# Kernel tuning notes

Measured on AMD Instinct MI355X. Metric: run time of the kernel, lower is better.

Reference implementation:

```python
import jax, jax.numpy as jnp
import numpy as np

IN_FEATURES = 4096
OUT_FEATURES = 4096
B, S = 4, 2048


def setup_inputs() -> dict:
    key = jax.random.key(0)
    k_x, k_w, k_ws, k_ss, k_b = jax.random.split(key, 5)
    x = jax.random.normal(k_x, (B, S, IN_FEATURES), dtype=jnp.float32)
    weight_quantized = jax.random.randint(k_w, (OUT_FEATURES, IN_FEATURES), -128, 128, dtype=jnp.int32).astype(jnp.int8)
    # realistic per-output-channel weight scales (small positive)
    weight_scale = jax.random.uniform(k_ws, (OUT_FEATURES,), dtype=jnp.float32, minval=1e-3, maxval=2e-2)
    # smoothing scales near 1 (clamped to [0.01, 100] in from_float)
    smooth_scale = jax.random.uniform(k_ss, (IN_FEATURES,), dtype=jnp.float32, minval=0.5, maxval=2.0)
    bias = 0.01 * jax.random.normal(k_b, (OUT_FEATURES,), dtype=jnp.float32)
    return {"x": x, "weight_quantized": weight_quantized, "weight_scale": weight_scale,
            "smooth_scale": smooth_scale, "bias": bias}


def reference(x, weight_quantized, weight_scale, smooth_scale, bias):
    # per-tensor dynamic activation quantization after smooth-scale divide
    x_smooth = x / smooth_scale                                   # [B,S,in]
    act_scale = jnp.max(jnp.abs(x_smooth)) / 127.0                # scalar
    x_quant = jnp.clip(jnp.round(x_smooth / (act_scale + 1e-5)), -128, 127).astype(jnp.int8)
    # int8 GEMM emulated in fp32 (matches torch reference: F.linear on float casts)
    out = jnp.einsum('bsi,oi->bso', x_quant.astype(jnp.float32),
                     weight_quantized.astype(jnp.float32))        # [B,S,out]
    out = out * act_scale * weight_scale                          # fused dequant
    return out + bias
```

## Files before the change

kernel.cpp:

```cpp
#include <hip/hip_runtime.h>
#include <stdint.h>

#define M_TOT 8192
#define N_TOT 4096
#define K_TOT 4096

typedef int v4i __attribute__((ext_vector_type(4)));
typedef int v16i __attribute__((ext_vector_type(16)));

#define BM 256
#define BN 256
#define SUB 64
#define NS (K_TOT / SUB)
#define A_SUB (BM * SUB)
#define B_SUB (BN * SUB)
#define BUF_BYTES (A_SUB + B_SUB)

__global__ void prep_reduce(const int4* __restrict__ w32, int* __restrict__ w8,
                            int nw4, const float4* __restrict__ smooth4,
                            const float4* __restrict__ x,
                            unsigned int* __restrict__ maxbits, int nx4) {
  const int stride = gridDim.x * blockDim.x;
  const int g0 = blockIdx.x * blockDim.x + threadIdx.x;
  for (int i = g0; i < nw4; i += stride) {
    int4 v = w32[i];
    w8[i] = (v.x & 0xff) | ((v.y & 0xff) << 8) | ((v.z & 0xff) << 16) | (v.w << 24);
  }
  float4 s = smooth4[g0 & (K_TOT / 4 - 1)];
  const float rx = 1.0f / s.x, ry = 1.0f / s.y, rz = 1.0f / s.z, rw = 1.0f / s.w;
  float m = 0.0f;
  for (int i = g0; i < nx4; i += stride) {
    float4 v = x[i];
    m = fmaxf(m, fabsf(v.x * rx));
    m = fmaxf(m, fabsf(v.y * ry));
    m = fmaxf(m, fabsf(v.z * rz));
    m = fmaxf(m, fabsf(v.w * rw));
  }
#pragma unroll
  for (int off = 32; off; off >>= 1) m = fmaxf(m, __shfl_xor(m, off));
  __shared__ float sm[4];
  if ((threadIdx.x & 63) == 0) sm[threadIdx.x >> 6] = m;
  __syncthreads();
  if (threadIdx.x == 0) {
    float mm = fmaxf(fmaxf(sm[0], sm[1]), fmaxf(sm[2], sm[3]));
    atomicMax(maxbits, __float_as_uint(mm));
  }
}

__global__ void quantize_x(const float4* __restrict__ x,
                           const float4* __restrict__ smooth4,
                           const unsigned int* __restrict__ maxbits,
                           int* __restrict__ xq, int n4) {
  const float d = __uint_as_float(*maxbits) / 127.0f + 1e-5f;
  const float inv = 1.0f / d;
  const int stride = gridDim.x * blockDim.x;
  const int g0 = blockIdx.x * blockDim.x + threadIdx.x;
  float4 s = smooth4[g0 & (K_TOT / 4 - 1)];
  const float rx = inv / s.x, ry = inv / s.y, rz = inv / s.z, rw = inv / s.w;
  for (int i = g0; i < n4; i += stride) {
    float4 v = x[i];
    int q0 = (int)fminf(fmaxf(rintf(v.x * rx), -128.0f), 127.0f);
    int q1 = (int)fminf(fmaxf(rintf(v.y * ry), -128.0f), 127.0f);
    int q2 = (int)fminf(fmaxf(rintf(v.z * rz), -128.0f), 127.0f);
    int q3 = (int)fminf(fmaxf(rintf(v.w * rw), -128.0f), 127.0f);
    xq[i] = (q0 & 0xff) | ((q1 & 0xff) << 8) | ((q2 & 0xff) << 16) | (q3 << 24);
  }
}

__global__ __launch_bounds__(512, 2) void gemm_i8(
    const int8_t* __restrict__ Aq,
    const int8_t* __restrict__ Wt,
    const unsigned int* __restrict__ maxbits,
    const float* __restrict__ wscale,
    const float* __restrict__ bias,
    float* __restrict__ out) {
  __shared__ int8_t lds[4 * BUF_BYTES];

  const int tid = threadIdx.x;
  const int lane = tid & 63;
  const int wid = tid >> 6;
  const int l31 = lane & 31;
  const int lhi5 = lane >> 5;

  const int flat = blockIdx.y * gridDim.x + blockIdx.x;
  const int swz = (flat & 7) * 64 + (flat >> 3);
  const int m0 = (swz / (N_TOT / BN)) * BM;
  const int n0 = (swz % (N_TOT / BN)) * BN;

  const int wave_m = wid >> 2;
  const int wave_n = wid & 3;

  const int row_l = lane >> 2;
  const int gcol = ((lane & 3) ^ ((lane >> 3) & 3)) << 4;
  const int8_t* Abase = Aq + (size_t)m0 * K_TOT;
  const int8_t* Bbase = Wt + (size_t)n0 * K_TOT;
  int goff[2];
#pragma unroll
  for (int c = 0; c < 2; ++c) {
    int grow = (wid * 2 + c) * 16 + row_l;
    goff[c] = grow * K_TOT + gcol;
  }

  auto stage = [&](int dstbuf, int koff) {
#pragma unroll
    for (int c = 0; c < 2; ++c) {
      __builtin_amdgcn_global_load_lds(
          (const __attribute__((address_space(1))) void*)(Abase + goff[c] + koff),
          (__attribute__((address_space(3))) void*)(lds + dstbuf * BUF_BYTES + (wid * 2 + c) * 1024),
          16, 0, 0);
      __builtin_amdgcn_global_load_lds(
          (const __attribute__((address_space(1))) void*)(Bbase + goff[c] + koff),
          (__attribute__((address_space(3))) void*)(lds + dstbuf * BUF_BYTES + A_SUB + (wid * 2 + c) * 1024),
          16, 0, 0);
    }
  };

  const int f = (l31 >> 1) & 3;
  const int slot0 = ((0 + lhi5) ^ f) << 4;
  const int slot1 = ((2 + lhi5) ^ f) << 4;
  const int aBase = (wave_m * 128 + l31) * SUB;
  const int bBase = (wave_n * 64 + l31) * SUB;

  stage(0, 0);
  stage(1, SUB);
  stage(2, 2 * SUB);
  asm volatile("s_waitcnt vmcnt(8)" ::: "memory");
  __builtin_amdgcn_s_barrier();
  __builtin_amdgcn_sched_barrier(0);

  v16i acc[4][2] = {};

#pragma unroll 4
  for (int s = 0; s < NS; ++s) {
    const int buf = s & 3;
    const int8_t* Ab = lds + buf * BUF_BYTES;
    const int8_t* Bb = Ab + A_SUB;

    const int ts = (s + 3 < NS) ? (s + 3) : (NS - 1);
    stage((s + 3) & 3, ts * SUB);

    v4i a0[4], a1[4], b0[2], b1[2];
#pragma unroll
    for (int mf = 0; mf < 4; ++mf) {
      a0[mf] = *(const v4i*)(Ab + aBase + mf * 2048 + slot0);
      a1[mf] = *(const v4i*)(Ab + aBase + mf * 2048 + slot1);
    }
#pragma unroll
    for (int nf = 0; nf < 2; ++nf) {
      b0[nf] = *(const v4i*)(Bb + bBase + nf * 2048 + slot0);
      b1[nf] = *(const v4i*)(Bb + bBase + nf * 2048 + slot1);
    }

    __builtin_amdgcn_s_setprio(1);
#pragma unroll
    for (int mf = 0; mf < 4; ++mf)
#pragma unroll
      for (int nf = 0; nf < 2; ++nf)
        acc[mf][nf] = __builtin_amdgcn_mfma_i32_32x32x32_i8(a0[mf], b0[nf], acc[mf][nf], 0, 0, 0);
#pragma unroll
    for (int mf = 0; mf < 4; ++mf)
#pragma unroll
      for (int nf = 0; nf < 2; ++nf)
        acc[mf][nf] = __builtin_amdgcn_mfma_i32_32x32x32_i8(a1[mf], b1[nf], acc[mf][nf], 0, 0, 0);
    __builtin_amdgcn_s_setprio(0);
    __builtin_amdgcn_sched_barrier(0);

    asm volatile("s_waitcnt lgkmcnt(0)" ::: "memory");
    asm volatile("s_waitcnt vmcnt(8)" ::: "memory");
    __builtin_amdgcn_sched_barrier(0);
    __builtin_amdgcn_s_barrier();
    __builtin_amdgcn_sched_barrier(0);
  }

  const float ascale = __uint_as_float(*maxbits) / 127.0f;
#pragma unroll
  for (int mf = 0; mf < 4; ++mf) {
#pragma unroll
    for (int nf = 0; nf < 2; ++nf) {
      const int ocol = n0 + wave_n * 64 + nf * 32 + l31;
      const float wsc = wscale[ocol] * ascale;
      const float bb = bias[ocol];
      const int rbase = m0 + wave_m * 128 + mf * 32 + 4 * lhi5;
#pragma unroll
      for (int reg = 0; reg < 16; ++reg) {
        const int orow = rbase + (reg & 3) + 8 * (reg >> 2);
        out[(size_t)orow * N_TOT + ocol] = (float)acc[mf][nf][reg] * wsc + bb;
      }
    }
  }
}

extern "C" void kernel_launch(void* const* d_in, const int* in_sizes, int n_in,
                              void* d_out, int out_size, void* d_ws, size_t ws_size,
                              hipStream_t stream) {
  const float* x = (const float*)d_in[0];
  const int* w32 = (const int*)d_in[1];
  const float* wscale = (const float*)d_in[2];
  const float* smooth = (const float*)d_in[3];
  const float* bias = (const float*)d_in[4];
  float* out = (float*)d_out;

  unsigned int* maxbits = (unsigned int*)d_ws;
  int8_t* xq = (int8_t*)d_ws + (1 << 20);
  int8_t* wq8 = xq + (size_t)M_TOT * K_TOT;

  hipMemsetAsync(d_ws, 0, 4, stream);

  const int nw4 = N_TOT * K_TOT / 4;
  const int n4 = M_TOT * K_TOT / 4;
  prep_reduce<<<2048, 256, 0, stream>>>((const int4*)w32, (int*)wq8, nw4,
                                        (const float4*)smooth, (const float4*)x,
                                        maxbits, n4);
  quantize_x<<<2048, 256, 0, stream>>>((const float4*)x, (const float4*)smooth,
                                       maxbits, (int*)xq, n4);

  dim3 grid(N_TOT / BN, M_TOT / BM);
  gemm_i8<<<grid, 512, 0, stream>>>(xq, wq8, maxbits, wscale, bias, out);
}
```

Baseline: 239.0 us.

## Load weight tiles directly to registers and switch to 16x16x64 int8 MFMA

```diff
diff --git a/kernel.cpp b/kernel.cpp
--- a/kernel.cpp
+++ b/kernel.cpp
@@ -6,15 +6,13 @@
 #define K_TOT 4096
 
 typedef int v4i __attribute__((ext_vector_type(4)));
-typedef int v16i __attribute__((ext_vector_type(16)));
 
 #define BM 256
 #define BN 256
 #define SUB 64
 #define NS (K_TOT / SUB)
 #define A_SUB (BM * SUB)
-#define B_SUB (BN * SUB)
-#define BUF_BYTES (A_SUB + B_SUB)
+#define BUF_BYTES A_SUB
 
 __global__ void prep_reduce(const int4* __restrict__ w32, int* __restrict__ w8,
                             int nw4, const float4* __restrict__ smooth4,
@@ -79,13 +77,14 @@
   const int tid = threadIdx.x;
   const int lane = tid & 63;
   const int wid = tid >> 6;
-  const int l31 = lane & 31;
-  const int lhi5 = lane >> 5;
+  const int l16 = lane & 15;
+  const int lhi = lane >> 4;
 
   const int flat = blockIdx.y * gridDim.x + blockIdx.x;
-  const int swz = (flat & 7) * 64 + (flat >> 3);
-  const int m0 = (swz / (N_TOT / BN)) * BM;
-  const int n0 = (swz % (N_TOT / BN)) * BN;
+  const int xcd = flat & 7;
+  const int idx = flat >> 3;
+  const int n0 = (xcd * 2 + (idx & 1)) * BN;
+  const int m0 = (idx >> 1) * BM;
 
   const int wave_m = wid >> 2;
   const int wave_n = wid & 3;
@@ -93,7 +92,6 @@
   const int row_l = lane >> 2;
   const int gcol = ((lane & 3) ^ ((lane >> 3) & 3)) << 4;
   const int8_t* Abase = Aq + (size_t)m0 * K_TOT;
-  const int8_t* Bbase = Wt + (size_t)n0 * K_TOT;
   int goff[2];
 #pragma unroll
   for (int c = 0; c < 2; ++c) {
@@ -108,83 +106,76 @@
           (const __attribute__((address_space(1))) void*)(Abase + goff[c] + koff),
           (__attribute__((address_space(3))) void*)(lds + dstbuf * BUF_BYTES + (wid * 2 + c) * 1024),
           16, 0, 0);
-      __builtin_amdgcn_global_load_lds(
-          (const __attribute__((address_space(1))) void*)(Bbase + goff[c] + koff),
-          (__attribute__((address_space(3))) void*)(lds + dstbuf * BUF_BYTES + A_SUB + (wid * 2 + c) * 1024),
-          16, 0, 0);
     }
   };
 
-  const int f = (l31 >> 1) & 3;
-  const int slot0 = ((0 + lhi5) ^ f) << 4;
-  const int slot1 = ((2 + lhi5) ^ f) << 4;
-  const int aBase = (wave_m * 128 + l31) * SUB;
-  const int bBase = (wave_n * 64 + l31) * SUB;
-
+  const int slot = (lhi ^ ((l16 >> 1) & 3)) << 4;
+  const int aOff = (wave_m * 128 + l16) * SUB + slot;
+
+  const int8_t* Bg = Wt + (size_t)(n0 + wave_n * 64 + l16) * K_TOT + lhi * 16;
+
+  v4i acc[8][4] = {};
+  v4i bE[4], bO[4];
+
+#pragma unroll
+  for (int j = 0; j < 4; ++j) bE[j] = *(const v4i*)(Bg + j * 16 * K_TOT);
+  __builtin_amdgcn_sched_barrier(0);
   stage(0, 0);
   stage(1, SUB);
   stage(2, 2 * SUB);
-  asm volatile("s_waitcnt vmcnt(8)" ::: "memory");
+  __builtin_amdgcn_sched_barrier(0);
+  asm volatile("s_waitcnt vmcnt(4)" ::: "memory");
   __builtin_amdgcn_s_barrier();
   __builtin_amdgcn_sched_barrier(0);
 
-  v16i acc[4][2] = {};
-
-#pragma unroll 4
-  for (int s = 0; s < NS; ++s) {
-    const int buf = s & 3;
-    const int8_t* Ab = lds + buf * BUF_BYTES;
-    const int8_t* Bb = Ab + A_SUB;
-
-    const int ts = (s + 3 < NS) ? (s + 3) : (NS - 1);
-    stage((s + 3) & 3, ts * SUB);
-
-    v4i a0[4], a1[4], b0[2], b1[2];
-#pragma unroll
-    for (int mf = 0; mf < 4; ++mf) {
-      a0[mf] = *(const v4i*)(Ab + aBase + mf * 2048 + slot0);
-      a1[mf] = *(const v4i*)(Ab + aBase + mf * 2048 + slot1);
-    }
-#pragma unroll
-    for (int nf = 0; nf < 2; ++nf) {
-      b0[nf] = *(const v4i*)(Bb + bBase + nf * 2048 + slot0);
-      b1[nf] = *(const v4i*)(Bb + bBase + nf * 2048 + slot1);
-    }
+  auto body = [&](int s, v4i (&cur)[4], v4i (&nxt)[4]) {
+    const int8_t* Ab = lds + (s & 3) * BUF_BYTES;
+
+    __builtin_amdgcn_sched_barrier(0);
+    const int kn = ((s + 1 < NS) ? s + 1 : NS - 1) * SUB;
+#pragma unroll
+    for (int j = 0; j < 4; ++j) nxt[j] = *(const v4i*)(Bg + j * 16 * K_TOT + kn);
+    __builtin_amdgcn_sched_barrier(0);
+    const int ts = ((s + 3 < NS) ? s + 3 : NS - 1) * SUB;
+    stage((s + 3) & 3, ts);
+    __builtin_amdgcn_sched_barrier(0);
+
+    v4i a[8];
+#pragma unroll
+    for (int i = 0; i < 8; ++i) a[i] = *(const v4i*)(Ab + aOff + i * 1024);
 
     __builtin_amdgcn_s_setprio(1);
 #pragma unroll
-    for (int mf = 0; mf < 4; ++mf)
-#pragma unroll
-      for (int nf = 0; nf < 2; ++nf)
-        acc[mf][nf] = __builtin_amdgcn_mfma_i32_32x32x32_i8(a0[mf], b0[nf], acc[mf][nf], 0, 0, 0);
-#pragma unroll
-    for (int mf = 0; mf < 4; ++mf)
-#pragma unroll
-      for (int nf = 0; nf < 2; ++nf)
-        acc[mf][nf] = __builtin_amdgcn_mfma_i32_32x32x32_i8(a1[mf], b1[nf], acc[mf][nf], 0, 0, 0);
+    for (int i = 0; i < 8; ++i)
+#pragma unroll
+      for (int j = 0; j < 4; ++j)
+        acc[i][j] = __builtin_amdgcn_mfma_i32_16x16x64_i8(a[i], cur[j], acc[i][j], 0, 0, 0);
     __builtin_amdgcn_s_setprio(0);
     __builtin_amdgcn_sched_barrier(0);
 
-    asm volatile("s_waitcnt lgkmcnt(0)" ::: "memory");
     asm volatile("s_waitcnt vmcnt(8)" ::: "memory");
     __builtin_amdgcn_sched_barrier(0);
     __builtin_amdgcn_s_barrier();
     __builtin_amdgcn_sched_barrier(0);
+  };
+
+  for (int s = 0; s < NS; s += 2) {
+    body(s, bE, bO);
+    body(s + 1, bO, bE);
   }
 
   const float ascale = __uint_as_float(*maxbits) / 127.0f;
 #pragma unroll
-  for (int mf = 0; mf < 4; ++mf) {
-#pragma unroll
-    for (int nf = 0; nf < 2; ++nf) {
-      const int ocol = n0 + wave_n * 64 + nf * 32 + l31;
+  for (int i = 0; i < 8; ++i) {
+    const int orow = m0 + wave_m * 128 + i * 16 + lhi * 4;
+#pragma unroll
+    for (int j = 0; j < 4; ++j) {
+      const int ocol = n0 + wave_n * 64 + j * 16 + l16;
       const float wsc = wscale[ocol] * ascale;
       const float bb = bias[ocol];
-      const int rbase = m0 + wave_m * 128 + mf * 32 + 4 * lhi5;
-#pragma unroll
-      for (int reg = 0; reg < 16; ++reg) {
-        const int orow = rbase + (reg & 3) + 8 * (reg >> 2);
-        out[(size_t)orow * N_TOT + ocol] = (float)acc[mf][nf][reg] * wsc + bb;
+#pragma unroll
+      for (int r = 0; r < 4; ++r) {
+        out[(size_t)(orow + r) * N_TOT + ocol] = (float)acc[i][j][r] * wsc + bb;
       }
     }
   }
```

Measured after the change: 281.6 us. +17.8%, slower.
